# Optimization experiments

Hardware: AMD Instinct MI355X
Metric: run time of the kernel (lower is better)

The kernel has to match this reference:

```python
import jax, jax.numpy as jnp
import numpy as np

N_NODES = 100000
N_EDGES = 1600000
C_IN = 128
C_OUT = 128


def setup_inputs() -> dict:
    key = jax.random.key(0)
    k1, k2, k3 = jax.random.split(key, 3)
    x = jax.random.normal(k1, (N_NODES, C_IN), dtype=jnp.float32)
    edge_index = jax.random.randint(k2, (2, N_EDGES), 0, N_NODES, dtype=jnp.int64)
    # Linear(in, out, bias=False) weight has shape [out, in]
    W = jax.random.normal(k3, (C_OUT, C_IN), dtype=jnp.float32) * 0.05
    return {"x": x, "edge_index": edge_index, "W": W}


def reference(x, edge_index, W):
    # Original builds dense A (adj[src,dst] += 1 per edge, counting duplicates),
    # adds self-loops I, computes d = A.sum(dim=0) (column sums = in-degree + 1),
    # then out = diag(1/d) @ A @ diag(1/d) @ (x @ W.T).
    # Equivalent edge-wise O(E) form:
    #   out[i] = (1/d[i]) * ( sum_{(i,j) in edges} h[j]/d[j]  +  h[i]/d[i] )
    N = x.shape[0]
    src, dst = edge_index[0], edge_index[1]
    # d[j] = (# edges with dst=j) + 1 (self-loop)
    deg = jax.ops.segment_sum(jnp.ones(src.shape[0], dtype=x.dtype), dst, num_segments=N) + 1.0
    h = x @ W.T                      # [N, C_out]
    hn = h / deg[:, None]            # h[j]/d[j]
    agg = jax.ops.segment_sum(hn[dst], src, num_segments=N) + hn  # neighbor msgs + self-loop
    return agg / deg[:, None]
```

## Files before the change

### kernel.cpp

```cpp
#include <hip/hip_runtime.h>
#include <hip/hip_bf16.h>

#define C 128
#define TPB 256
#define TPB3 1024
#define BWID 512
#define NBUK 256
#define PADB 9472

typedef __attribute__((ext_vector_type(8))) _Float16 half8;
typedef __attribute__((ext_vector_type(4))) float f32x4;
typedef __attribute__((ext_vector_type(2))) float fv2;
typedef __attribute__((ext_vector_type(2))) int iv2;
typedef __attribute__((ext_vector_type(2))) long long ll2;
typedef unsigned long long u64;

#define OFF_CURS  0x400
#define OFF_CURD  0xC00
#define OFF_OFFS  0xA0000
#define OFF_CNTS  0x110000
#define OFF_INVD  0x180000
#define OFF_EDST  0x200000
#define OFF_HN    0xC00000

__device__ __forceinline__ unsigned f2bf_bits(float f) {
    unsigned u = __float_as_uint(f);
    return (u + 0x7fffu + ((u >> 16) & 1u)) >> 16;
}

__global__ void init_kernel(int* __restrict__ gcurS, int* __restrict__ gcurD) {
    const int t = threadIdx.x;
    gcurS[t] = t * PADB;
    gcurD[t] = t * PADB;
}

__global__ __launch_bounds__(TPB3) void scatter2_kernel(const void* __restrict__ edges,
                                                        long long E, int chunk,
                                                        int* __restrict__ gcurS,
                                                        int* __restrict__ gcurD,
                                                        u64* __restrict__ partS,
                                                        int* __restrict__ partD) {
    __shared__ int flag_s;
    __shared__ int hs[NBUK], hd[NBUK];
    __shared__ int cs[NBUK], cd[NBUK];
    const int t = threadIdx.x;
    const int B = blockIdx.x;
    if (t == 0) flag_s = 0;
    if (t < NBUK) { hs[t] = 0; hd[t] = 0; }
    __syncthreads();
    {
        const unsigned* ew = (const unsigned*)edges;
        int any = 0;
        for (int k = t; k < 2048; k += TPB3) {
            const long long widx = 2LL * k + 1;
            if (widx < 2 * E) any |= (ew[widx] != 0u);
        }
        if (any) atomicOr(&flag_s, 1);
    }
    __syncthreads();
    const int is32 = flag_s;
    const int Eeven = ((E & 1) == 0);
    const long long b0 = (long long)B * chunk;

    for (int i = 2 * t; i < chunk; i += 2 * TPB3) {
        const long long e0 = b0 + i;
        const bool v0 = (e0 < E);
        const bool v1 = (i + 1 < chunk) && (e0 + 1 < E);
        int s0 = 0, d0 = 0, s1 = 0, d1 = 0;
        if (is32) {
            const int* p = (const int*)edges;
            if (v0 && v1 && Eeven) {
                const iv2 sv = *(const iv2*)(p + e0);
                const iv2 dv = *(const iv2*)(p + E + e0);
                s0 = sv.x; s1 = sv.y; d0 = dv.x; d1 = dv.y;
            } else {
                if (v0) { s0 = p[e0]; d0 = p[E + e0]; }
                if (v1) { s1 = p[e0 + 1]; d1 = p[E + e0 + 1]; }
            }
        } else {
            const long long* p = (const long long*)edges;
            if (v0 && v1 && Eeven) {
                const ll2 sv = *(const ll2*)(p + e0);
                const ll2 dv = *(const ll2*)(p + E + e0);
                s0 = (int)sv.x; s1 = (int)sv.y; d0 = (int)dv.x; d1 = (int)dv.y;
            } else {
                if (v0) { s0 = (int)p[e0]; d0 = (int)p[E + e0]; }
                if (v1) { s1 = (int)p[e0 + 1]; d1 = (int)p[E + e0 + 1]; }
            }
        }
        if (v0) { atomicAdd(&hs[s0 >> 9], 1); atomicAdd(&hd[d0 >> 9], 1); }
        if (v1) { atomicAdd(&hs[s1 >> 9], 1); atomicAdd(&hd[d1 >> 9], 1); }
    }
    __syncthreads();

    if (t < NBUK) {
        cs[t] = atomicAdd(&gcurS[t], hs[t]);
        cd[t] = atomicAdd(&gcurD[t], hd[t]);
    }
    __syncthreads();

    for (int i = 2 * t; i < chunk; i += 2 * TPB3) {
        const long long e0 = b0 + i;
        const bool v0 = (e0 < E);
        const bool v1 = (i + 1 < chunk) && (e0 + 1 < E);
        int s0 = 0, d0 = 0, s1 = 0, d1 = 0;
        if (is32) {
            const int* p = (const int*)edges;
            if (v0 && v1 && Eeven) {
                const iv2 sv = *(const iv2*)(p + e0);
                const iv2 dv = *(const iv2*)(p + E + e0);
                s0 = sv.x; s1 = sv.y; d0 = dv.x; d1 = dv.y;
            } else {
                if (v0) { s0 = p[e0]; d0 = p[E + e0]; }
                if (v1) { s1 = p[e0 + 1]; d1 = p[E + e0 + 1]; }
            }
        } else {
            const long long* p = (const long long*)edges;
            if (v0 && v1 && Eeven) {
                const ll2 sv = *(const ll2*)(p + e0);
                const ll2 dv = *(const ll2*)(p + E + e0);
                s0 = (int)sv.x; s1 = (int)sv.y; d0 = (int)dv.x; d1 = (int)dv.y;
            } else {
                if (v0) { s0 = (int)p[e0]; d0 = (int)p[E + e0]; }
                if (v1) { s1 = (int)p[e0 + 1]; d1 = (int)p[E + e0 + 1]; }
            }
        }
        if (v0) {
            const int ps = atomicAdd(&cs[s0 >> 9], 1);
            partS[ps] = ((u64)(unsigned)d0 << 32) | (unsigned)s0;
            const int pd = atomicAdd(&cd[d0 >> 9], 1);
            partD[pd] = d0;
        }
        if (v1) {
            const int ps = atomicAdd(&cs[s1 >> 9], 1);
            partS[ps] = ((u64)(unsigned)d1 << 32) | (unsigned)s1;
            const int pd = atomicAdd(&cd[d1 >> 9], 1);
            partD[pd] = d1;
        }
    }
}

__global__ __launch_bounds__(TPB3) void csrdeg_kernel(const u64* __restrict__ partS,
                                                      const int* __restrict__ partD,
                                                      const int* __restrict__ gcurS,
                                                      const int* __restrict__ gcurD,
                                                      int* __restrict__ offS,
                                                      int* __restrict__ cntS,
                                                      int* __restrict__ eDst,
                                                      float* __restrict__ invd, int N) {
    __shared__ int cnt[BWID], off[BWID];
    __shared__ int wtot[16];
    const int t = threadIdx.x;
    const int B = blockIdx.x;
    const int lo = B * BWID;
    if (lo >= N) return;
    const int wv = t >> 6, ln = t & 63;
    const int eb = B * PADB, ee = gcurS[B];
    if (t < BWID) cnt[t] = 0;
    __syncthreads();
    for (int e = eb + t; e < ee; e += TPB3)
        atomicAdd(&cnt[(int)(partS[e] & 0xffffffffu) - lo], 1);
    __syncthreads();
    const int loc = (t < BWID) ? cnt[t] : 0;
    int v = loc;
#pragma unroll
    for (int d = 1; d < 64; d <<= 1) {
        const int n = __shfl_up(v, d);
        if (ln >= d) v += n;
    }
    if (ln == 63) wtot[wv] = v;
    __syncthreads();
    if (wv == 0) {
        const int wv_ = (ln < 16) ? wtot[ln] : 0;
        int w2 = wv_;
#pragma unroll
        for (int d = 1; d < 16; d <<= 1) {
            const int n = __shfl_up(w2, d);
            if (ln >= d) w2 += n;
        }
        if (ln < 16) wtot[ln] = w2 - wv_;
    }
    __syncthreads();
    const int ex = v - loc + wtot[wv];
    if (t < BWID) {
        off[t] = ex;
        const int node = lo + t;
        if (node < N) { offS[node] = eb + ex; cntS[node] = loc; }
    }
    __syncthreads();
    for (int e = eb + t; e < ee; e += TPB3) {
        const u64 p = partS[e];
        const int sv = (int)(p & 0xffffffffu);
        const int dv = (int)(p >> 32);
        const int pos = atomicAdd(&off[sv - lo], 1);
        eDst[eb + pos] = dv;
    }
    __syncthreads();
    if (t < BWID) cnt[t] = 0;
    __syncthreads();
    const int db = B * PADB, de = gcurD[B];
    for (int e = db + t; e < de; e += TPB3)
        atomicAdd(&cnt[partD[e] - lo], 1);
    __syncthreads();
    if (t < BWID) {
        const int node = lo + t;
        if (node < N) invd[node] = 1.0f / (float)(cnt[t] + 1);
    }
}

__global__ __launch_bounds__(TPB) void gemm_mfma_kernel(const float* __restrict__ x,
                                                        const float* __restrict__ W,
                                                        const float* __restrict__ invd,
                                                        unsigned short* __restrict__ hn,
                                                        int N) {
    __shared__ _Float16 Wl[C * C];
    const int t = threadIdx.x;
    const int lane = t & 63;
    const int wid = t >> 6;
    const int lr = lane & 15;
    const int lk = lane >> 4;
    const int m0 = blockIdx.x * 128 + wid * 32;

    {
        const float4* W4 = (const float4*)W;
#pragma unroll
        for (int i = 0; i < 16; ++i) {
            const int g = i * TPB + t;
            const float4 v = W4[g];
            const int row = g >> 5;
            const int c4 = g & 31;
            const int chunk = c4 >> 1;
            const int half = c4 & 1;
            union { _Float16 h[4]; unsigned long long u; } p;
            p.h[0] = (_Float16)v.x; p.h[1] = (_Float16)v.y;
            p.h[2] = (_Float16)v.z; p.h[3] = (_Float16)v.w;
            const int off = row * 256 + ((chunk ^ (row & 7)) << 4) + (half << 3);
            *(unsigned long long*)((char*)Wl + off) = p.u;
        }
    }

    half8 a[2][4];
#pragma unroll
    for (int mb = 0; mb < 2; ++mb) {
        const int row = m0 + mb * 16 + lr;
        const float* xp = x + (size_t)row * C + lk * 8;
#pragma unroll
        for (int ks = 0; ks < 4; ++ks) {
            half8 av;
            if (row < N) {
                const float4 v0 = *(const float4*)(xp + ks * 32);
                const float4 v1 = *(const float4*)(xp + ks * 32 + 4);
                av[0] = (_Float16)v0.x; av[1] = (_Float16)v0.y;
                av[2] = (_Float16)v0.z; av[3] = (_Float16)v0.w;
                av[4] = (_Float16)v1.x; av[5] = (_Float16)v1.y;
                av[6] = (_Float16)v1.z; av[7] = (_Float16)v1.w;
            } else {
                av = (half8)((_Float16)0.f);
            }
            a[mb][ks] = av;
        }
    }
    __syncthreads();

    f32x4 acc[2][8];
#pragma unroll
    for (int mb = 0; mb < 2; ++mb)
#pragma unroll
        for (int nf = 0; nf < 8; ++nf)
            acc[mb][nf] = (f32x4){0.f, 0.f, 0.f, 0.f};

#pragma unroll
    for (int nf = 0; nf < 8; ++nf) {
        const int brow = nf * 16 + lr;
        half8 b[4];
#pragma unroll
        for (int ks = 0; ks < 4; ++ks) {
            const int chunkp = (lk + ks * 4) ^ (lr & 7);
            b[ks] = *(const half8*)((const char*)Wl + brow * 256 + chunkp * 16);
        }
#pragma unroll
        for (int mb = 0; mb < 2; ++mb)
#pragma unroll
            for (int ks = 0; ks < 4; ++ks)
                acc[mb][nf] = __builtin_amdgcn_mfma_f32_16x16x32_f16(
                    a[mb][ks], b[ks], acc[mb][nf], 0, 0, 0);
    }

#pragma unroll
    for (int mb = 0; mb < 2; ++mb) {
#pragma unroll
        for (int r = 0; r < 4; ++r) {
            const int row = m0 + mb * 16 + lk * 4 + r;
            if (row < N) {
                const float idv = invd[row];
                unsigned short* hp = hn + (size_t)row * C + lr;
#pragma unroll
                for (int nf = 0; nf < 8; ++nf)
                    hp[nf * 16] = (unsigned short)f2bf_bits(acc[mb][nf][r] * idv);
            }
        }
    }
}

__global__ __launch_bounds__(TPB) void gather_kernel(const int* __restrict__ offS,
                                                     const int* __restrict__ cntS,
                                                     const int* __restrict__ eDst,
                                                     const uint4* __restrict__ hnb4,
                                                     const float* __restrict__ invd,
                                                     float* __restrict__ out, int N) {
    const int lane = threadIdx.x & 63;
    const int w = (blockIdx.x * TPB + threadIdx.x) >> 6;
    if (w >= N) return;
    const int sub = lane >> 4;
    const int ll  = lane & 15;
    const int beg = offS[w];
    const int cnt = cntS[w];
    const int total = cnt + 1;

    float acc[8];
#pragma unroll
    for (int i = 0; i < 8; ++i) acc[i] = 0.f;

    for (int j0 = 0; j0 < total; j0 += 64) {
        const int m = min(64, total - j0);
        int dl = w;
        if (lane < m && j0 + lane < cnt)
            dl = __builtin_nontemporal_load(&eDst[beg + j0 + lane]);
#pragma unroll 4
        for (int q = 0; q < m; q += 4) {
            const int d = __shfl(dl, q + sub);
            if (q + sub < m) {
                const uint4 v = hnb4[(size_t)d * 16 + ll];
                acc[0] += __uint_as_float(v.x << 16);
                acc[1] += __uint_as_float(v.x & 0xffff0000u);
                acc[2] += __uint_as_float(v.y << 16);
                acc[3] += __uint_as_float(v.y & 0xffff0000u);
                acc[4] += __uint_as_float(v.z << 16);
                acc[5] += __uint_as_float(v.z & 0xffff0000u);
                acc[6] += __uint_as_float(v.w << 16);
                acc[7] += __uint_as_float(v.w & 0xffff0000u);
            }
        }
    }

#pragma unroll
    for (int i = 0; i < 8; ++i) {
        acc[i] += __shfl_xor(acc[i], 16);
        acc[i] += __shfl_xor(acc[i], 32);
    }

    const float s = invd[w];
    fv2 o;
    o.x = acc[sub * 2] * s;
    o.y = acc[sub * 2 + 1] * s;
    fv2* op = (fv2*)(out + (size_t)w * C + ll * 8 + sub * 2);
    __builtin_nontemporal_store(o, op);
}

extern "C" void kernel_launch(void* const* d_in, const int* in_sizes, int n_in,
                              void* d_out, int out_size, void* d_ws, size_t ws_size,
                              hipStream_t stream) {
    const float* x = (const float*)d_in[0];
    const void* edges = d_in[1];
    const float* W = (const float*)d_in[2];
    float* out = (float*)d_out;

    const int N = in_sizes[0] / C;
    const long long E = (long long)in_sizes[1] / 2;

    char* ws = (char*)d_ws;
    int*       gcurS = (int*)(ws + OFF_CURS);
    int*       gcurD = (int*)(ws + OFF_CURD);
    int*       offS  = (int*)(ws + OFF_OFFS);
    int*       cntS  = (int*)(ws + OFF_CNTS);
    float*     invd  = (float*)(ws + OFF_INVD);
    int*       eDst  = (int*)(ws + OFF_EDST);
    unsigned short* hn = (unsigned short*)(ws + OFF_HN);

    int* o32   = (int*)d_out;
    u64* partS = (u64*)o32;
    int* partD = o32 + 2 * NBUK * PADB;

    const int chunk = (int)((E + NBUK - 1) / NBUK);

    init_kernel<<<1, NBUK, 0, stream>>>(gcurS, gcurD);
    scatter2_kernel<<<NBUK, TPB3, 0, stream>>>(edges, E, chunk, gcurS, gcurD,
                                               partS, partD);
    csrdeg_kernel<<<NBUK, TPB3, 0, stream>>>(partS, partD, gcurS, gcurD,
                                             offS, cntS, eDst, invd, N);

    const int nBlkG = (N + 127) / 128;
    gemm_mfma_kernel<<<nBlkG, TPB, 0, stream>>>(x, W, invd, hn, N);

    const int nBlkA = (N * 64 + TPB - 1) / TPB;
    gather_kernel<<<nBlkA, TPB, 0, stream>>>(offS, cntS, eDst, (const uint4*)hn,
                                             invd, out, N);
}
```

Baseline: 136.0 us.

## Pack bucketed edge records tighter and stage GEMM output through LDS

The per-bucket edge records shrink from 64-bit to 32-bit words, storing a 9-bit local source and a 17-bit destination. The degree bucket entries shrink from int to 16-bit local indices. This cuts global traffic in the scatter and CSR-build kernels. The GEMM epilogue now writes bf16 results into swizzled shared memory and then emits coalesced 16-byte row stores instead of scattered 2-byte stores. The packing assumes node ids fit in 17 bits and buckets are 512 nodes wide.

Result: slower. 140.9 us (+3.6%).

```diff
diff --git a/kernel.cpp b/kernel.cpp
--- a/kernel.cpp
+++ b/kernel.cpp
@@ -13,7 +13,6 @@
 typedef __attribute__((ext_vector_type(2))) float fv2;
 typedef __attribute__((ext_vector_type(2))) int iv2;
 typedef __attribute__((ext_vector_type(2))) long long ll2;
-typedef unsigned long long u64;
 
 #define OFF_CURS  0x400
 #define OFF_CURD  0xC00
@@ -38,8 +37,8 @@
                                                         long long E, int chunk,
                                                         int* __restrict__ gcurS,
                                                         int* __restrict__ gcurD,
-                                                        u64* __restrict__ partS,
-                                                        int* __restrict__ partD) {
+                                                        unsigned* __restrict__ partS,
+                                                        unsigned short* __restrict__ partD) {
     __shared__ int flag_s;
     __shared__ int hs[NBUK], hd[NBUK];
     __shared__ int cs[NBUK], cd[NBUK];
@@ -127,21 +126,21 @@
         }
         if (v0) {
             const int ps = atomicAdd(&cs[s0 >> 9], 1);
-            partS[ps] = ((u64)(unsigned)d0 << 32) | (unsigned)s0;
+            partS[ps] = ((unsigned)(s0 & 511) << 17) | (unsigned)d0;
             const int pd = atomicAdd(&cd[d0 >> 9], 1);
-            partD[pd] = d0;
+            partD[pd] = (unsigned short)(d0 & 511);
         }
         if (v1) {
             const int ps = atomicAdd(&cs[s1 >> 9], 1);
-            partS[ps] = ((u64)(unsigned)d1 << 32) | (unsigned)s1;
+            partS[ps] = ((unsigned)(s1 & 511) << 17) | (unsigned)d1;
             const int pd = atomicAdd(&cd[d1 >> 9], 1);
-            partD[pd] = d1;
-        }
-    }
-}
-
-__global__ __launch_bounds__(TPB3) void csrdeg_kernel(const u64* __restrict__ partS,
-                                                      const int* __restrict__ partD,
+            partD[pd] = (unsigned short)(d1 & 511);
+        }
+    }
+}
+
+__global__ __launch_bounds__(TPB3) void csrdeg_kernel(const unsigned* __restrict__ partS,
+                                                      const unsigned short* __restrict__ partD,
                                                       const int* __restrict__ gcurS,
                                                       const int* __restrict__ gcurD,
                                                       int* __restrict__ offS,
@@ -159,7 +158,7 @@
     if (t < BWID) cnt[t] = 0;
     __syncthreads();
     for (int e = eb + t; e < ee; e += TPB3)
-        atomicAdd(&cnt[(int)(partS[e] & 0xffffffffu) - lo], 1);
+        atomicAdd(&cnt[partS[e] >> 17], 1);
     __syncthreads();
     const int loc = (t < BWID) ? cnt[t] : 0;
     int v = loc;
@@ -189,10 +188,10 @@
     }
     __syncthreads();
     for (int e = eb + t; e < ee; e += TPB3) {
-        const u64 p = partS[e];
-        const int sv = (int)(p & 0xffffffffu);
-        const int dv = (int)(p >> 32);
-        const int pos = atomicAdd(&off[sv - lo], 1);
+        const unsigned p = partS[e];
+        const int lsrc = (int)(p >> 17);
+        const int dv = (int)(p & 0x1FFFFu);
+        const int pos = atomicAdd(&off[lsrc], 1);
         eDst[eb + pos] = dv;
     }
     __syncthreads();
@@ -200,7 +199,7 @@
     __syncthreads();
     const int db = B * PADB, de = gcurD[B];
     for (int e = db + t; e < de; e += TPB3)
-        atomicAdd(&cnt[partD[e] - lo], 1);
+        atomicAdd(&cnt[partD[e]], 1);
     __syncthreads();
     if (t < BWID) {
         const int node = lo + t;
@@ -286,17 +285,36 @@
                     a[mb][ks], b[ks], acc[mb][nf], 0, 0, 0);
     }
 
+    __syncthreads();
+    unsigned short* ob = (unsigned short*)Wl;
 #pragma unroll
     for (int mb = 0; mb < 2; ++mb) {
 #pragma unroll
         for (int r = 0; r < 4; ++r) {
-            const int row = m0 + mb * 16 + lk * 4 + r;
-            if (row < N) {
-                const float idv = invd[row];
-                unsigned short* hp = hn + (size_t)row * C + lr;
-#pragma unroll
-                for (int nf = 0; nf < 8; ++nf)
-                    hp[nf * 16] = (unsigned short)f2bf_bits(acc[mb][nf][r] * idv);
+            const int lrow = wid * 32 + mb * 16 + lk * 4 + r;
+            const int grow = blockIdx.x * 128 + lrow;
+            if (grow < N) {
+                const float idv = invd[grow];
+#pragma unroll
+                for (int nf = 0; nf < 8; ++nf) {
+                    const int col = nf * 16 + lr;
+                    const int phys = (col >> 3) ^ (lrow & 15);
+                    ob[lrow * 128 + phys * 8 + (col & 7)] =
+                        (unsigned short)f2bf_bits(acc[mb][nf][r] * idv);
+                }
+            }
+        }
+    }
+    __syncthreads();
+    {
+        const int orow = t >> 1, oh = t & 1;
+        const int grow = blockIdx.x * 128 + orow;
+        if (grow < N) {
+            uint4* dst = (uint4*)(hn + (size_t)grow * C + oh * 64);
+#pragma unroll
+            for (int j = 0; j < 8; ++j) {
+                const int phys = (oh * 8 + j) ^ (orow & 15);
+                dst[j] = *(const uint4*)(ob + orow * 128 + phys * 8);
             }
         }
     }
@@ -377,16 +395,16 @@
     int*       eDst  = (int*)(ws + OFF_EDST);
     unsigned short* hn = (unsigned short*)(ws + OFF_HN);
 
-    int* o32   = (int*)d_out;
-    u64* partS = (u64*)o32;
-    int* partD = o32 + 2 * NBUK * PADB;
+    int* o32 = (int*)d_out;
+    unsigned*       partS   = (unsigned*)o32;
+    unsigned short* partD16 = (unsigned short*)(o32 + NBUK * PADB);
 
     const int chunk = (int)((E + NBUK - 1) / NBUK);
 
     init_kernel<<<1, NBUK, 0, stream>>>(gcurS, gcurD);
     scatter2_kernel<<<NBUK, TPB3, 0, stream>>>(edges, E, chunk, gcurS, gcurD,
-                                               partS, partD);
-    csrdeg_kernel<<<NBUK, TPB3, 0, stream>>>(partS, partD, gcurS, gcurD,
+                                               partS, partD16);
+    csrdeg_kernel<<<NBUK, TPB3, 0, stream>>>(partS, partD16, gcurS, gcurD,
                                              offS, cntS, eDst, invd, N);
 
     const int nBlkG = (N + 127) / 128;
```
